# Kernel optimization log

Hardware: AMD Instinct MI355X
Metric: run time of the kernel (lower is better)

The kernel has to match this reference:

```python
import jax, jax.numpy as jnp
import numpy as np

L = 512          # profile HMM model length (number of match states)
S = 25           # alphabet size (input_dim)
BATCH = 128
T_LEN = 1024
TINY = np.finfo(np.float32).tiny


def setup_inputs():
    key = jax.random.key(0)
    ks = jax.random.split(key, 18)
    def n(k, shape):
        return 0.1 * jax.random.normal(k, shape, dtype=jnp.float32)
    return {
        "seq": jax.random.randint(ks[0], (BATCH, T_LEN), 0, S),
        "em_kernel": n(ks[1], (L, S)),
        "ins_kernel": n(ks[2], (S,)),
        "flank_kernel": n(ks[3], (1,)),
        "btm": n(ks[4], (L,)),
        "m2e": n(ks[5], (L,)),
        "mtm": n(ks[6], (L - 1,)),
        "m2i": n(ks[7], (L - 1,)),
        "i2m": n(ks[8], (L - 1,)),
        "i2i": n(ks[9], (L - 1,)),
        "mtd": n(ks[10], (L,)),
        "dtm": n(ks[11], (L,)),
        "dtd": n(ks[12], (L - 1,)),
        "lf_loop": n(ks[13], (1,)),
        "lf_exit": n(ks[14], (1,)),
        "e2u": n(ks[15], (1,)),
        "e2r": n(ks[16], (1,)),
        "e2t": n(ks[17], (1,)),
    }


def _build_hmm(em_kernel, ins_kernel, flank_kernel, btm, m2e, mtm, m2i, i2m, i2i,
               mtd, dtm, dtd, lf_loop, lf_exit, e2u, e2r, e2t):
    """Build implicit transition matrix A [q,q], emission matrix B [q,S+1], init dist [q].
    Explicit states begin/end/delete are marginalized out (silent states), yielding the
    implicit transition structure of the profile HMM (match skips via delete chains)."""
    Lm = em_kernel.shape[0]
    q = 2 * Lm + 3                      # LF, M_1..M_L, I_1..I_{L-1}, U, RF, T
    U, RF, TM = 2 * Lm, 2 * Lm + 1, 2 * Lm + 2
    idx = jnp.arange(Lm)
    dt = em_kernel.dtype
    # per-source-state softmax over explicit outgoing edges
    begin_p = jax.nn.softmax(jnp.concatenate([btm, mtd[:1]]))            # begin -> M_j / D_1
    btm_p = begin_p[:Lm]
    mp = jax.nn.softmax(jnp.stack([mtm, m2i, m2e[:Lm - 1], mtd[1:]], axis=-1), axis=-1)
    mtm_p, m2i_p, m2e_p, mtd_mid = mp[:, 0], mp[:, 1], mp[:, 2], mp[:, 3]
    ip = jax.nn.softmax(jnp.stack([i2m, i2i], axis=-1), axis=-1)
    i2m_p, i2i_p = ip[:, 0], ip[:, 1]
    dp = jax.nn.softmax(jnp.stack([dtm[:Lm - 1], dtd], axis=-1), axis=-1)
    dtm_p = jnp.concatenate([dp[:, 0], jnp.ones((1,), dt)])              # D_L -> end with prob 1
    dtd_p = dp[:, 1]
    fp = jax.nn.softmax(jnp.concatenate([lf_loop, lf_exit]))            # shared flank kernels
    floop, fexit = fp[0], fp[1]
    ep = jax.nn.softmax(jnp.concatenate([e2u, e2r, e2t]))               # end -> U / RF / T
    # marginalize silent delete chain. Sk[i,k]: P(src_i => target via deletes),
    # src_0 = begin, src_i = M_i; target M_{k+2} for k<=L-2, end for k=L-1.
    mtd_p = jnp.concatenate([begin_p[Lm:], mtd_mid])                    # begin->D_1, M_i->D_{i+1}
    cp_log = jnp.concatenate([jnp.zeros((1,), dt), jnp.cumsum(jnp.log(dtd_p))])
    Sk = mtd_p[:, None] * jnp.exp(cp_log[None, :] - cp_log[:, None]) * dtm_p[None, :]
    Sk = jnp.where(idx[None, :] >= idx[:, None], Sk, jnp.zeros((), dt))
    enter = btm_p + jnp.pad(Sk[0, :Lm - 1], (1, 0))                      # begin => M_j
    begin_end = Sk[0, Lm - 1]                                            # begin => end (all deleted)
    m2e_tot = jnp.concatenate([m2e_p + Sk[1:, Lm - 1], jnp.ones((1,), dt)])
    A = jnp.zeros((q, q), dt)
    Mblk = jnp.zeros((Lm, Lm), dt).at[idx[:-1], idx[1:]].set(mtm_p)
    Mblk = Mblk.at[0:Lm - 1, 1:Lm].add(Sk[1:Lm, 0:Lm - 1])               # match skips (j>=i+2)
    A = A.at[1:Lm + 1, 1:Lm + 1].set(Mblk)
    A = A.at[0, 0].set(floop)
    A = A.at[0, 1:Lm + 1].set(fexit * enter)
    A = A.at[0, U].set(fexit * begin_end * ep[0])
    A = A.at[0, RF].set(fexit * begin_end * ep[1])
    A = A.at[0, TM].set(fexit * begin_end * ep[2])
    A = A.at[jnp.arange(1, Lm), jnp.arange(Lm + 1, 2 * Lm)].set(m2i_p)   # M_i -> I_i
    A = A.at[1:Lm + 1, U].set(m2e_tot * ep[0])
    A = A.at[1:Lm + 1, RF].set(m2e_tot * ep[1])
    A = A.at[1:Lm + 1, TM].set(m2e_tot * ep[2])
    A = A.at[jnp.arange(Lm + 1, 2 * Lm), jnp.arange(2, Lm + 1)].set(i2m_p)  # I_i -> M_{i+1}
    A = A.at[jnp.arange(Lm + 1, 2 * Lm), jnp.arange(Lm + 1, 2 * Lm)].set(i2i_p)
    A = A.at[U, 1:Lm + 1].set(fexit * enter)
    A = A.at[U, U].set(floop + fexit * begin_end * ep[0])
    A = A.at[U, RF].set(fexit * begin_end * ep[1])
    A = A.at[U, TM].set(fexit * begin_end * ep[2])
    A = A.at[RF, RF].set(floop)
    A = A.at[RF, TM].set(fexit)
    A = A.at[TM, TM].set(1.0)
    # emission matrix per make_default_emission_matrix: [ins; em; ins x (L+1)] rows,
    # softmax, zero pad column, terminal one-hot row -> [2L+3, S+1]
    rows = jnp.concatenate([ins_kernel[None], em_kernel,
                            jnp.tile(ins_kernel[None], (Lm + 1, 1))], axis=0)
    Bm = jax.nn.softmax(rows, axis=-1)
    Bm = jnp.concatenate([Bm, jnp.zeros((2 * Lm + 2, 1), dt)], axis=-1)
    s_alph = em_kernel.shape[1]
    Bm = jnp.concatenate([Bm, jax.nn.one_hot(jnp.array([s_alph]), s_alph + 1, dtype=dt)], axis=0)
    # initial distribution: start in left flank w.p. sigmoid(flank_init), else enter model
    p0 = jax.nn.sigmoid(flank_kernel[0])
    init = jnp.zeros((q,), dt).at[0].set(p0)
    init = init.at[1:Lm + 1].set((1 - p0) * enter)
    init = init.at[U].set((1 - p0) * begin_end * ep[0])
    init = init.at[RF].set((1 - p0) * begin_end * ep[1])
    init = init.at[TM].set((1 - p0) * begin_end * ep[2])
    return A, Bm, init


def _forward(seq, *params):
    A, Bm, init = _build_hmm(*params)
    # emission probs per timestep: matvec(B, one_hot(x)) == column gather
    E = Bm.T[seq]                        # [batch, T, q]
    alpha = init[None, :] * E[:, 0]
    s = alpha.sum(-1, keepdims=True) + TINY
    ll = jnp.log(s[:, 0])
    alpha = alpha / s

    def step(carry, Et):
        a, l = carry
        a = Et * (a @ A)                 # forward-algorithm recurrence + scaling
        sn = a.sum(-1, keepdims=True) + TINY
        return (a / sn, l + jnp.log(sn[:, 0])), None

    (alpha, ll), _ = jax.lax.scan(step, (alpha, ll), jnp.swapaxes(E[:, 1:], 0, 1))
    return ll                            # [batch] sequence log-likelihoods


def reference(seq, em_kernel, ins_kernel, flank_kernel, btm, m2e, mtm, m2i, i2m, i2i,
              mtd, dtm, dtd, lf_loop, lf_exit, e2u, e2r, e2t):
    return _forward(seq, em_kernel, ins_kernel, flank_kernel, btm, m2e, mtm, m2i, i2m,
                    i2i, mtd, dtm, dtd, lf_loop, lf_exit, e2u, e2r, e2t)
```

## Files before the change

kernel.cpp:

```cpp
#include <hip/hip_runtime.h>
#include <math.h>

#define LM 512
#define TLEN 1024
#define TINY_F 1.17549435e-38f

#define OFF_ENTER 0
#define OFF_MTM   512
#define OFF_I2M   1024
#define OFF_DTM   1536
#define OFF_WC    2048
#define OFF_MC    2560
#define OFF_M2I   3072
#define OFF_I2I   3584
#define OFF_M2E   4096
#define OFF_INS   4608
#define OFF_SC    4640
#define OFF_EMB   5120

typedef float v2f __attribute__((ext_vector_type(2)));

__device__ __forceinline__ v2f pfma(v2f a, v2f b, v2f c) {
    return __builtin_elementwise_fma(a, b, c);
}
__device__ __forceinline__ v2f vs(float c) { return (v2f){c, c}; }

template<int Ctrl, int RowMask>
__device__ __forceinline__ float fdpp(float oldv, float src) {
    int r = __builtin_amdgcn_update_dpp(
        __builtin_bit_cast(int, oldv), __builtin_bit_cast(int, src),
        Ctrl, RowMask, 0xF, false);
    return __builtin_bit_cast(float, r);
}

__device__ __forceinline__ float rdlane63(float v) {
    return __builtin_bit_cast(float,
        __builtin_amdgcn_readlane(__builtin_bit_cast(int, v), 63));
}

__device__ __forceinline__ float wave_sum_to63(float v) {
    v += fdpp<0x111, 0xF>(0.f, v);
    v += fdpp<0x112, 0xF>(0.f, v);
    v += fdpp<0x114, 0xF>(0.f, v);
    v += fdpp<0x118, 0xF>(0.f, v);
    v += fdpp<0x142, 0xA>(0.f, v);
    v += fdpp<0x143, 0xC>(0.f, v);
    return v;
}

__global__ __launch_bounds__(512) void hmm_setup(
    const float* __restrict__ em, const float* __restrict__ ins,
    const float* __restrict__ flank, const float* __restrict__ btm,
    const float* __restrict__ m2e, const float* __restrict__ mtm,
    const float* __restrict__ m2i, const float* __restrict__ i2m,
    const float* __restrict__ i2i, const float* __restrict__ mtd,
    const float* __restrict__ dtm, const float* __restrict__ dtd,
    const float* __restrict__ lfl, const float* __restrict__ lfe,
    const float* __restrict__ e2u, const float* __restrict__ e2r,
    const float* __restrict__ e2t, float* __restrict__ P)
{
    __shared__ float beginp[513];
    __shared__ float mtdp[512], dtmp[512], dtdp[512], cplog[512];
    __shared__ float mtmp[512], m2ip[512], m2ep[512], i2mp[512], i2ip[512];
    __shared__ float rbuf[512], rbuf2[512];
    __shared__ float inspS[25];
    const int j = threadIdx.x;

    if (j < 25) {
        float sm = 0.f;
        for (int s = 0; s < 25; ++s) sm += expf(ins[s]);
        inspS[j] = expf(ins[j]) / sm;
        P[OFF_INS + j] = log2f(inspS[j]);
    }

    float eb = expf(btm[j]);
    rbuf[j] = eb;
    __syncthreads();
    for (int s = 256; s > 0; s >>= 1) {
        if (j < s) rbuf[j] += rbuf[j + s];
        __syncthreads();
    }
    float e512 = expf(mtd[0]);
    float tot = rbuf[0] + e512;
    beginp[j] = eb / tot;
    if (j == 0) { beginp[512] = e512 / tot; mtdp[0] = e512 / tot; }

    if (j < 511) {
        float a = expf(mtm[j]), b = expf(m2i[j]), c = expf(m2e[j]), d = expf(mtd[j + 1]);
        float s = a + b + c + d;
        mtmp[j] = a / s; m2ip[j] = b / s; m2ep[j] = c / s; mtdp[j + 1] = d / s;
        float ia = expf(i2m[j]), ib = expf(i2i[j]); s = ia + ib;
        i2mp[j] = ia / s; i2ip[j] = ib / s;
        float da = expf(dtm[j]), db = expf(dtd[j]); s = da + db;
        dtmp[j] = da / s; dtdp[j] = db / s;
    }
    if (j == 511) dtmp[511] = 1.0f;
    __syncthreads();

    {
        float lw = (j >= 1) ? logf(dtdp[j - 1]) : 0.f;
        rbuf[j] = lw;
        __syncthreads();
        float* bufs[2] = { rbuf, rbuf2 };
        int cur = 0;
        for (int off = 1; off < 512; off <<= 1) {
            float v = bufs[cur][j];
            if (j >= off) v += bufs[cur][j - off];
            bufs[cur ^ 1][j] = v;
            cur ^= 1;
            __syncthreads();
        }
        cplog[j] = bufs[cur][j];
    }
    __syncthreads();

    if (j == 0) {
        float fl = expf(lfl[0]), fe = expf(lfe[0]); float fs = fl + fe;
        float floop = fl / fs, fexit = fe / fs;
        float eu = expf(e2u[0]), er = expf(e2r[0]), et = expf(e2t[0]);
        float es = eu + er + et; float ep0 = eu / es, ep1 = er / es;
        float p0 = 1.0f / (1.0f + expf(-flank[0]));
        P[OFF_SC + 0] = floop;
        P[OFF_SC + 1] = fexit;
        P[OFF_SC + 2] = p0;
        P[OFF_SC + 5] = ep0;
        P[OFF_SC + 6] = ep1;
        P[OFF_SC + 9] = 1.0f - p0;
    }
    __syncthreads();

    float en = beginp[j];
    if (j >= 1) en += mtdp[0] * expf(cplog[j - 1]) * dtmp[j - 1];
    P[OFF_ENTER + j] = en;
    P[OFF_MTM + j] = (j >= 1) ? mtmp[j - 1] : 0.f;
    P[OFF_I2M + j] = (j >= 1) ? i2mp[j - 1] : 0.f;
    P[OFF_DTM + j] = (j >= 1) ? dtmp[j - 1] : 0.f;
    P[OFF_WC  + j] = (j >= 1) ? mtdp[j]     : 0.f;
    P[OFF_MC  + j] = (j >= 1) ? dtdp[j - 1] : 0.f;
    P[OFF_M2I + j] = (j < 511) ? m2ip[j] : 0.f;
    P[OFF_I2I + j] = (j < 511) ? i2ip[j] : 0.f;
    P[OFF_M2E + j] = (j < 511)
        ? (m2ep[j] + mtdp[j + 1] * expf(cplog[511] - cplog[j + 1]))
        : 1.0f;

    {
        const float* row = em + j * 25;
        float mx = row[0];
        for (int s = 1; s < 25; ++s) mx = fmaxf(mx, row[s]);
        float sm = 0.f;
        for (int s = 0; s < 25; ++s) sm += expf(row[s] - mx);
        float inv = 1.0f / sm;
        int lanej = j >> 3, e = j & 7;
        int pos = ((e >> 2) << 8) | (lanej << 2) | (e & 3);
        for (int s = 0; s < 25; ++s)
            P[OFF_EMB + s * 512 + pos] = (expf(row[s] - mx) * inv) / inspS[s];
    }
}

__global__ __launch_bounds__(64, 1) void hmm_forward(
    const int* __restrict__ seq, const float* __restrict__ P,
    float* __restrict__ out)
{
    __shared__ __align__(16) float sEmb[25 * 512];
    __shared__ float sLogEi[32];
    __shared__ __align__(16) int sSeq[TLEN + 4];

    const int lane = threadIdx.x;
    const int b = blockIdx.x;
    const int base = lane * 8;

    {
        const float4* src = (const float4*)(P + OFF_EMB);
        float4* dst = (float4*)sEmb;
#pragma unroll 5
        for (int k = lane; k < 25 * 128; k += 64) dst[k] = src[k];
        if (lane < 32) sLogEi[lane] = P[OFF_INS + (lane < 25 ? lane : 0)];
        const int4* s4 = (const int4*)(seq + b * TLEN);
        int4* d4 = (int4*)sSeq;
#pragma unroll
        for (int k = lane; k < 256; k += 64) d4[k] = s4[k];
        if (lane < 4) sSeq[TLEN + lane] = 0;
    }
    __syncthreads();

    float llE;
    {
        float le = 0.f;
#pragma unroll
        for (int k = 0; k < 16; ++k) le += sLogEi[sSeq[lane * 16 + k]];
        llE = rdlane63(wave_sum_to63(le));
    }

    float mtm_[8], dtm_[8], wC_[8], mC_[8];
    v2f enter2[4], m2iS2[4], i2i2[4], m2e2[4], dtmM2[4], invNX2[4];
    {
        float enter_[8], m2iS_[8], i2i_[8], m2e_[8], dtmM_[8], invNX_[8];
#pragma unroll
        for (int e = 0; e < 8; ++e) {
            enter_[e] = P[OFF_ENTER + base + e];
            mtm_[e]   = P[OFF_MTM + base + e];
            dtm_[e]   = P[OFF_DTM + base + e];
            wC_[e]    = P[OFF_WC + base + e];
            mC_[e]    = P[OFF_MC + base + e];
            i2i_[e]   = P[OFF_I2I + base + e];
            m2e_[e]   = P[OFF_M2E + base + e];
            float i2mN = (base + e + 1 < 512) ? P[OFF_I2M + base + e + 1] : 1.0f;
            m2iS_[e]  = P[OFF_M2I + base + e] * i2mN;
            invNX_[e] = 1.0f / i2mN;
        }
        float Mp = mC_[0];
        dtmM_[0] = dtm_[0];
#pragma unroll
        for (int e = 1; e < 8; ++e) { dtmM_[e] = dtm_[e] * Mp; Mp *= mC_[e]; }
#pragma unroll
        for (int p = 0; p < 4; ++p) {
            enter2[p] = (v2f){enter_[2*p], enter_[2*p+1]};
            m2iS2[p]  = (v2f){m2iS_[2*p],  m2iS_[2*p+1]};
            i2i2[p]   = (v2f){i2i_[2*p],   i2i_[2*p+1]};
            m2e2[p]   = (v2f){m2e_[2*p],   m2e_[2*p+1]};
            dtmM2[p]  = (v2f){dtmM_[2*p],  dtmM_[2*p+1]};
            invNX2[p] = (v2f){invNX_[2*p], invNX_[2*p+1]};
        }
    }
    const float floop = P[OFF_SC + 0], fexit = P[OFF_SC + 1], p0 = P[OFF_SC + 2];
    const float ep0 = P[OFF_SC + 5], ep1 = P[OFF_SC + 6];
    const float omp0 = P[OFF_SC + 9];

    v2f am2[4], ci2[4];
#define AM(e) ((e) & 1 ? am2[(e) >> 1].y : am2[(e) >> 1].x)
#define CI(e) ((e) & 1 ? ci2[(e) >> 1].y : ci2[(e) >> 1].x)

    v2f EmA2[4], EmB2[4];
    {
        int s0 = sSeq[0];
        const float4* c4 = (const float4*)(sEmb + (s0 << 9) + (lane << 2));
        float4 xx = c4[0], yy = c4[64];
        EmA2[0] = (v2f){xx.x, xx.y}; EmA2[1] = (v2f){xx.z, xx.w};
        EmA2[2] = (v2f){yy.x, yy.y}; EmA2[3] = (v2f){yy.z, yy.w};
    }
#pragma unroll
    for (int p = 0; p < 4; ++p) {
        am2[p] = EmA2[p] * vs(omp0) * enter2[p];
        ci2[p] = (v2f){0.f, 0.f};
    }
    float f0 = p0;
    float U  = 0.f;
    float RF = 0.f;
    float ll2 = llE;

    int symN = sSeq[1];
    {
        const float4* c4 = (const float4*)(sEmb + (symN << 9) + (lane << 2));
        float4 xx = c4[0], yy = c4[64];
        EmA2[0] = (v2f){xx.x, xx.y}; EmA2[1] = (v2f){xx.z, xx.w};
        EmA2[2] = (v2f){yy.x, yy.y}; EmA2[3] = (v2f){yy.z, yy.w};
    }
    symN = sSeq[2];
    int sidx = 3;

#define STEP(EmC2, EmN2, DO_NORM)                                              \
  {                                                                            \
    {                \
      const float4* c4 = (const float4*)(sEmb + (symN << 9) + (lane << 2));    \
      float4 xx = c4[0], yy = c4[64];                                          \
      EmN2[0] = (v2f){xx.x, xx.y}; EmN2[1] = (v2f){xx.z, xx.w};                \
      EmN2[2] = (v2f){yy.x, yy.y}; EmN2[3] = (v2f){yy.z, yy.w};                \
      symN = sSeq[sidx]; ++sidx;                                               \
    }                                                                          \
    float amL = fdpp<0x138, 0xF>(0.f, am2[3].y);                               \
    float ciL = fdpp<0x138, 0xF>(0.f, ci2[3].y);                               \
                 \
    float Apre[8];                                                             \
    Apre[0] = amL * wC_[0];                                                    \
    _Pragma("unroll")                                                          \
    for (int e = 1; e < 8; ++e)                                                \
      Apre[e] = fmaf(Apre[e - 1], mC_[e], AM(e - 1) * wC_[e]);                 \
         \
    float carry = fdpp<0x138, 0xF>(0.f, Apre[7]);                              \
                \
    v2f dv = am2[0] * m2e2[0];                                                 \
    dv = pfma(am2[1], m2e2[1], dv);                                            \
    dv = pfma(am2[2], m2e2[2], dv);                                            \
    dv = pfma(am2[3], m2e2[3], dv);                                            \
    float dsum = rdlane63(wave_sum_to63(dv.x + dv.y));                         \
                     \
    float aFU = (f0 + U) * fexit;                                              \
    f0 = f0 * floop;                                                           \
    U  = fmaf(dsum, ep0, U * floop);                                           \
    RF = fmaf(dsum, ep1, RF * floop);                                          \
       \
    v2f tp[4];                                                                 \
    tp[0].x = fmaf(amL, mtm_[0], ciL);                                         \
    tp[0].y = fmaf(AM(0), mtm_[1], CI(0));                                     \
    tp[1].x = fmaf(AM(1), mtm_[2], CI(1));                                     \
    tp[1].y = fmaf(AM(2), mtm_[3], CI(2));                                     \
    tp[2].x = fmaf(AM(3), mtm_[4], CI(3));                                     \
    tp[2].y = fmaf(AM(4), mtm_[5], CI(4));                                     \
    tp[3].x = fmaf(AM(5), mtm_[6], CI(5));                                     \
    tp[3].y = fmaf(AM(6), mtm_[7], CI(6));                                     \
                       \
    ci2[0] = pfma(am2[0], m2iS2[0], ci2[0] * i2i2[0]);                         \
    ci2[1] = pfma(am2[1], m2iS2[1], ci2[1] * i2i2[1]);                         \
    ci2[2] = pfma(am2[2], m2iS2[2], ci2[2] * i2i2[2]);                         \
    ci2[3] = pfma(am2[3], m2iS2[3], ci2[3] * i2i2[3]);                         \
      \
    v2f aFU2 = vs(aFU), carry2 = vs(carry);                                    \
    tp[0] = pfma(aFU2, enter2[0], tp[0]);                                      \
    tp[1] = pfma(aFU2, enter2[1], tp[1]);                                      \
    tp[2] = pfma(aFU2, enter2[2], tp[2]);                                      \
    tp[3] = pfma(aFU2, enter2[3], tp[3]);                                      \
    tp[0].y = fmaf(dtm_[1], Apre[0], tp[0].y);                                 \
    tp[1].x = fmaf(dtm_[2], Apre[1], tp[1].x);                                 \
    tp[1].y = fmaf(dtm_[3], Apre[2], tp[1].y);                                 \
    tp[2].x = fmaf(dtm_[4], Apre[3], tp[2].x);                                 \
    tp[2].y = fmaf(dtm_[5], Apre[4], tp[2].y);                                 \
    tp[3].x = fmaf(dtm_[6], Apre[5], tp[3].x);                                 \
    tp[3].y = fmaf(dtm_[7], Apre[6], tp[3].y);                                 \
    tp[0] = pfma(dtmM2[0], carry2, tp[0]);                                     \
    tp[1] = pfma(dtmM2[1], carry2, tp[1]);                                     \
    tp[2] = pfma(dtmM2[2], carry2, tp[2]);                                     \
    tp[3] = pfma(dtmM2[3], carry2, tp[3]);                                     \
    am2[0] = EmC2[0] * tp[0];                                                  \
    am2[1] = EmC2[1] * tp[1];                                                  \
    am2[2] = EmC2[2] * tp[2];                                                  \
    am2[3] = EmC2[3] * tp[3];                                                  \
      \
                                      \
    if (DO_NORM) {                                                             \
      v2f ns = pfma(ci2[0], invNX2[0], am2[0]);                                \
      ns += pfma(ci2[1], invNX2[1], am2[1]);                                   \
      ns += pfma(ci2[2], invNX2[2], am2[2]);                                   \
      ns += pfma(ci2[3], invNX2[3], am2[3]);                                   \
      float sl = ns.x + ns.y + ((lane == 0) ? (f0 + U + RF) : 0.f);            \
      float s = rdlane63(wave_sum_to63(sl)) + TINY_F;                          \
      ll2 += __log2f(s);                                                       \
      float inv = 1.0f / s;                                                    \
      v2f inv2 = vs(inv);                                                      \
      am2[0] *= inv2; am2[1] *= inv2; am2[2] *= inv2; am2[3] *= inv2;          \
      ci2[0] *= inv2; ci2[1] *= inv2; ci2[2] *= inv2; ci2[3] *= inv2;          \
      f0 *= inv; U *= inv; RF *= inv;                                          \
    }                                                                          \
  }

#define PAIR(NORM2)                                                            \
    STEP(EmA2, EmB2, 0)                                                        \
    STEP(EmB2, EmA2, NORM2)

    for (int c = 0; c < 63; ++c) {
        int nf = ((c & 3) == 3);
        PAIR(0) PAIR(0) PAIR(0) PAIR(0)
        PAIR(0) PAIR(0) PAIR(0) PAIR(nf)
    }
    for (int p = 0; p < 7; ++p) {
        PAIR(0)
    }
    STEP(EmA2, EmB2, 1)
#undef PAIR
#undef STEP
#undef AM
#undef CI

    if (lane == 0) out[b] = ll2 * 0.69314718055994530942f;
}

extern "C" void kernel_launch(void* const* d_in, const int* in_sizes, int n_in,
                              void* d_out, int out_size, void* d_ws, size_t ws_size,
                              hipStream_t stream) {
    const int*   seq   = (const int*)d_in[0];
    const float* em    = (const float*)d_in[1];
    const float* ins   = (const float*)d_in[2];
    const float* flank = (const float*)d_in[3];
    const float* btm   = (const float*)d_in[4];
    const float* m2e   = (const float*)d_in[5];
    const float* mtm   = (const float*)d_in[6];
    const float* m2i   = (const float*)d_in[7];
    const float* i2m   = (const float*)d_in[8];
    const float* i2i   = (const float*)d_in[9];
    const float* mtd   = (const float*)d_in[10];
    const float* dtm   = (const float*)d_in[11];
    const float* dtd   = (const float*)d_in[12];
    const float* lfl   = (const float*)d_in[13];
    const float* lfe   = (const float*)d_in[14];
    const float* e2u   = (const float*)d_in[15];
    const float* e2r   = (const float*)d_in[16];
    const float* e2t   = (const float*)d_in[17];
    float* P = (float*)d_ws;
    float* out = (float*)d_out;

    hipLaunchKernelGGL(hmm_setup, dim3(1), dim3(512), 0, stream,
        em, ins, flank, btm, m2e, mtm, m2i, i2m, i2i, mtd, dtm, dtd,
        lfl, lfe, e2u, e2r, e2t, P);
    hipLaunchKernelGGL(hmm_forward, dim3(128), dim3(64), 0, stream, seq, P, out);
}
```

Before: 263.4 us.

## Split emission setup into separate kernel, pack flank states, use bound-ctrl DPP

Moves the emission-ratio table computation out of the single-block setup kernel into its own 8-block kernel, so that work is spread across several workgroups instead of one. In the forward loop, the flank state bookkeeping (f0 merged with U, plus RF) is packed into one two-wide vector updated with a packed FMA. The lane-shift DPP ops switch to bound_ctrl with a zero old value, which may save a register move. The extra kernel launch adds some launch overhead.

```diff
diff --git a/kernel.cpp b/kernel.cpp
--- a/kernel.cpp
+++ b/kernel.cpp
@@ -33,6 +33,14 @@
     return __builtin_bit_cast(float, r);
 }
 
+template<int Ctrl, int RowMask>
+__device__ __forceinline__ float fdppb(float src) {
+    int r = __builtin_amdgcn_update_dpp(
+        0, __builtin_bit_cast(int, src),
+        Ctrl, RowMask, 0xF, true);
+    return __builtin_bit_cast(float, r);
+}
+
 __device__ __forceinline__ float rdlane63(float v) {
     return __builtin_bit_cast(float,
         __builtin_amdgcn_readlane(__builtin_bit_cast(int, v), 63));
@@ -49,7 +57,7 @@
 }
 
 __global__ __launch_bounds__(512) void hmm_setup(
-    const float* __restrict__ em, const float* __restrict__ ins,
+    const float* __restrict__ ins,
     const float* __restrict__ flank, const float* __restrict__ btm,
     const float* __restrict__ m2e, const float* __restrict__ mtm,
     const float* __restrict__ m2i, const float* __restrict__ i2m,
@@ -63,14 +71,12 @@
     __shared__ float mtdp[512], dtmp[512], dtdp[512], cplog[512];
     __shared__ float mtmp[512], m2ip[512], m2ep[512], i2mp[512], i2ip[512];
     __shared__ float rbuf[512], rbuf2[512];
-    __shared__ float inspS[25];
     const int j = threadIdx.x;
 
     if (j < 25) {
         float sm = 0.f;
         for (int s = 0; s < 25; ++s) sm += expf(ins[s]);
-        inspS[j] = expf(ins[j]) / sm;
-        P[OFF_INS + j] = log2f(inspS[j]);
+        P[OFF_INS + j] = log2f(expf(ins[j]) / sm);
     }
 
     float eb = expf(btm[j]);
@@ -142,18 +148,29 @@
     P[OFF_M2E + j] = (j < 511)
         ? (m2ep[j] + mtdp[j + 1] * expf(cplog[511] - cplog[j + 1]))
         : 1.0f;
-
-    {
-        const float* row = em + j * 25;
-        float mx = row[0];
-        for (int s = 1; s < 25; ++s) mx = fmaxf(mx, row[s]);
-        float sm = 0.f;
-        for (int s = 0; s < 25; ++s) sm += expf(row[s] - mx);
-        float inv = 1.0f / sm;
-        int lanej = j >> 3, e = j & 7;
-        int pos = ((e >> 2) << 8) | (lanej << 2) | (e & 3);
-        for (int s = 0; s < 25; ++s)
-            P[OFF_EMB + s * 512 + pos] = (expf(row[s] - mx) * inv) / inspS[s];
+}
+
+__global__ __launch_bounds__(64) void hmm_emrel(
+    const float* __restrict__ em, const float* __restrict__ ins,
+    float* __restrict__ P)
+{
+    const int j = blockIdx.x * 64 + threadIdx.x;
+
+    float sm = 0.f;
+    for (int s = 0; s < 25; ++s) sm += expf(ins[s]);
+
+    const float* row = em + j * 25;
+    float mx = row[0];
+    for (int s = 1; s < 25; ++s) mx = fmaxf(mx, row[s]);
+    float sme = 0.f;
+    for (int s = 0; s < 25; ++s) sme += expf(row[s] - mx);
+    float inv = 1.0f / sme;
+
+    int lanej = j >> 3, e = j & 7;
+    int pos = ((e >> 2) << 8) | (lanej << 2) | (e & 3);
+    for (int s = 0; s < 25; ++s) {
+        float inspS = expf(ins[s]) / sm;
+        P[OFF_EMB + s * 512 + pos] = (expf(row[s] - mx) * inv) / inspS;
     }
 }
 
@@ -225,6 +242,8 @@
     const float floop = P[OFF_SC + 0], fexit = P[OFF_SC + 1], p0 = P[OFF_SC + 2];
     const float ep0 = P[OFF_SC + 5], ep1 = P[OFF_SC + 6];
     const float omp0 = P[OFF_SC + 9];
+    const v2f floop2 = vs(floop);
+    const v2f epv2 = (v2f){ep0, ep1};
 
     v2f am2[4], ci2[4];
 #define AM(e) ((e) & 1 ? am2[(e) >> 1].y : am2[(e) >> 1].x)
@@ -243,9 +262,7 @@
         am2[p] = EmA2[p] * vs(omp0) * enter2[p];
         ci2[p] = (v2f){0.f, 0.f};
     }
-    float f0 = p0;
-    float U  = 0.f;
-    float RF = 0.f;
+    v2f GR = (v2f){p0, 0.f};
     float ll2 = llE;
 
     int symN = sSeq[1];
@@ -267,8 +284,8 @@
       EmN2[2] = (v2f){yy.x, yy.y}; EmN2[3] = (v2f){yy.z, yy.w};                \
       symN = sSeq[sidx]; ++sidx;                                               \
     }                                                                          \
-    float amL = fdpp<0x138, 0xF>(0.f, am2[3].y);                               \
-    float ciL = fdpp<0x138, 0xF>(0.f, ci2[3].y);                               \
+    float amL = fdppb<0x138, 0xF>(am2[3].y);                                   \
+    float ciL = fdppb<0x138, 0xF>(ci2[3].y);                                   \
                  \
     float Apre[8];                                                             \
     Apre[0] = amL * wC_[0];                                                    \
@@ -276,18 +293,16 @@
     for (int e = 1; e < 8; ++e)                                                \
       Apre[e] = fmaf(Apre[e - 1], mC_[e], AM(e - 1) * wC_[e]);                 \
          \
-    float carry = fdpp<0x138, 0xF>(0.f, Apre[7]);                              \
+    float carry = fdppb<0x138, 0xF>(Apre[7]);                                  \
                 \
     v2f dv = am2[0] * m2e2[0];                                                 \
     dv = pfma(am2[1], m2e2[1], dv);                                            \
     dv = pfma(am2[2], m2e2[2], dv);                                            \
     dv = pfma(am2[3], m2e2[3], dv);                                            \
     float dsum = rdlane63(wave_sum_to63(dv.x + dv.y));                         \
-                     \
-    float aFU = (f0 + U) * fexit;                                              \
-    f0 = f0 * floop;                                                           \
-    U  = fmaf(dsum, ep0, U * floop);                                           \
-    RF = fmaf(dsum, ep1, RF * floop);                                          \
+              \
+    float aFU = GR.x * fexit;                                                  \
+    GR = pfma(vs(dsum), epv2, GR * floop2);                                    \
        \
     v2f tp[4];                                                                 \
     tp[0].x = fmaf(amL, mtm_[0], ciL);                                         \
@@ -331,14 +346,14 @@
       ns += pfma(ci2[1], invNX2[1], am2[1]);                                   \
       ns += pfma(ci2[2], invNX2[2], am2[2]);                                   \
       ns += pfma(ci2[3], invNX2[3], am2[3]);                                   \
-      float sl = ns.x + ns.y + ((lane == 0) ? (f0 + U + RF) : 0.f);            \
+      float sl = ns.x + ns.y + ((lane == 0) ? (GR.x + GR.y) : 0.f);            \
       float s = rdlane63(wave_sum_to63(sl)) + TINY_F;                          \
       ll2 += __log2f(s);                                                       \
       float inv = 1.0f / s;                                                    \
       v2f inv2 = vs(inv);                                                      \
       am2[0] *= inv2; am2[1] *= inv2; am2[2] *= inv2; am2[3] *= inv2;          \
       ci2[0] *= inv2; ci2[1] *= inv2; ci2[2] *= inv2; ci2[3] *= inv2;          \
-      f0 *= inv; U *= inv; RF *= inv;                                          \
+      GR *= inv2;                                                              \
     }                                                                          \
   }
 
@@ -387,8 +402,9 @@
     float* P = (float*)d_ws;
     float* out = (float*)d_out;
 
+    hipLaunchKernelGGL(hmm_emrel, dim3(8), dim3(64), 0, stream, em, ins, P);
     hipLaunchKernelGGL(hmm_setup, dim3(1), dim3(512), 0, stream,
-        em, ins, flank, btm, m2e, mtm, m2i, i2m, i2i, mtd, dtm, dtd,
+        ins, flank, btm, m2e, mtm, m2i, i2m, i2i, mtd, dtm, dtd,
         lfl, lfe, e2u, e2r, e2t, P);
     hipLaunchKernelGGL(hmm_forward, dim3(128), dim3(64), 0, stream, seq, P, out);
 }
```

New measurement: 256.7 us. -2.5%, faster.
